# Performance work log

Hardware: AMD Instinct MI355X
Metric: run time of the kernel (lower is better)

The kernel has to match this reference:

```python
import jax, jax.numpy as jnp
import numpy as np


def setup_inputs() -> dict:
    key = jax.random.key(0)
    k1, k2 = jax.random.split(key)
    B, S, H, E = 4, 8192, 4096, 64
    x = jax.random.normal(k1, (B, S, H), dtype=jnp.float32)
    # gate weight [E, H], scaled like a standard init_method
    weight = jax.random.normal(k2, (E, H), dtype=jnp.float32) * (H ** -0.5)
    expert_biases = jnp.zeros((E,), dtype=jnp.float32)
    return {"x": x, "weight": weight, "expert_biases": expert_biases, "top_k": 8}


def reference(x, weight, expert_biases, top_k):
    BIAS_UPDATE_RATE = 0.01
    batch_shape = x.shape[:-1]
    E, H = weight.shape
    flat_x = x.reshape(-1, H)            # [N, H]
    n_tokens = flat_x.shape[0]

    raw_scores = flat_x @ weight.T       # [N, E] gate GEMM
    probs = jax.nn.softmax(raw_scores + expert_biases, axis=-1)  # biased softmax

    expert_weights, expert_indices = jax.lax.top_k(probs, top_k)  # [N, K]

    # bincount with fixed length E (jit-friendly scatter-add)
    token_counts = jnp.zeros((E,), jnp.int32).at[expert_indices.reshape(-1)].add(1)

    # loss-free balancing bias update (training-time buffer update)
    tokens_per_expert = n_tokens * top_k / E
    load_violations = token_counts.astype(jnp.float32) - tokens_per_expert
    new_expert_biases = expert_biases + BIAS_UPDATE_RATE * jnp.sign(load_violations)

    scores = probs.reshape(*batch_shape, E)
    expert_weights = expert_weights.reshape(*batch_shape, top_k)
    expert_indices = expert_indices.reshape(*batch_shape, top_k)
    return (scores, expert_weights, expert_indices, new_expert_biases)
```

## Files before the change

kernel.cpp:

```cpp
#include <hip/hip_runtime.h>

#define NE 64
#define TAU 1e-4f
#define LSTR 68

typedef __bf16 bf16x8 __attribute__((ext_vector_type(8)));
typedef float f32x4 __attribute__((ext_vector_type(4)));

__device__ __forceinline__ void split8(const float4 a0, const float4 a1,
                                       bf16x8& hi, bf16x8& lo) {
  const float xs[8] = {a0.x, a0.y, a0.z, a0.w, a1.x, a1.y, a1.z, a1.w};
#pragma unroll
  for (int i = 0; i < 8; ++i) {
    const __bf16 h = (__bf16)xs[i];
    hi[i] = h;
    lo[i] = (__bf16)(xs[i] - (float)h);
  }
}

__device__ __forceinline__ void gld16(const void* g, void* l) {
  __builtin_amdgcn_global_load_lds(
      (const __attribute__((address_space(1))) void*)g,
      (__attribute__((address_space(3))) void*)l, 16, 0, 0);
}

__global__ void zero512(int* __restrict__ p) { p[threadIdx.x] = 0; }

__global__ __launch_bounds__(256) void wconvert(const float* __restrict__ W,
                                                __bf16* __restrict__ Whi,
                                                __bf16* __restrict__ Wlo,
                                                int n8, int H) {
  const int i = blockIdx.x * 256 + threadIdx.x;
  if (i >= n8) return;
  const int hc = H >> 3;
  const int e = i / hc;
  const int k0 = (i - e * hc) * 8;
  const float4 a0 = *reinterpret_cast<const float4*>(W + (size_t)e * H + k0);
  const float4 a1 =
      *reinterpret_cast<const float4*>(W + (size_t)e * H + k0 + 4);
  bf16x8 hi, lo;
  split8(a0, a1, hi, lo);
  const int tt = k0 >> 5, lk = (k0 >> 3) & 3, j = e >> 4, lr = e & 15;
  const size_t off = (size_t)tt * 2048 + j * 512 + (lk * 16 + lr) * 8;
  *reinterpret_cast<bf16x8*>(Whi + off) = hi;
  *reinterpret_cast<bf16x8*>(Wlo + off) = lo;
}

__global__ __launch_bounds__(512, 2) void gemm_fused(
    const float* __restrict__ X, const __bf16* __restrict__ Whi,
    const __bf16* __restrict__ Wlo, const float* __restrict__ bias,
    float* __restrict__ S, float* __restrict__ wout, float* __restrict__ iout,
    int* __restrict__ cnt, int* __restrict__ hist, int* __restrict__ list,
    int cap, int H, int K) {
  __shared__ alignas(16) char smem[131072];
  __shared__ int hist_s[NE];
  const int tid = threadIdx.x;
  const int lane = tid & 63;
  const int wave = tid >> 6;
  if (tid < NE) hist_s[tid] = 0;
  const int lr = lane & 15;
  const int lk = lane >> 4;
  const int row0 = blockIdx.x * 128;

  __bf16* BH = (__bf16*)smem;
  __bf16* BL = (__bf16*)(smem + 65536);

  const float* xp = X + (size_t)(row0 + 16 * wave + lr) * H + 8 * lk;
  const int T = (H >> 5);
  const int NSL = T >> 4;

  f32x4 acc[4] = {};
  float4 aC0 = *reinterpret_cast<const float4*>(xp);
  float4 aC1 = *reinterpret_cast<const float4*>(xp + 4);

  for (int s = 0; s < NSL; ++s) {
    if (s) __syncthreads();
    const __bf16* sh = Whi + (size_t)s * 32768 + wave * 4096 + lane * 8;
    const __bf16* sl = Wlo + (size_t)s * 32768 + wave * 4096 + lane * 8;
#pragma unroll
    for (int i = 0; i < 8; ++i) {
      gld16(sh + i * 512, BH + wave * 4096 + i * 512);
      gld16(sl + i * 512, BL + wave * 4096 + i * 512);
    }
    asm volatile("s_waitcnt vmcnt(0)" ::: "memory");
    __syncthreads();

#pragma unroll 4
    for (int st = 0; st < 16; ++st) {
      const int t = s * 16 + st;
      const int tn = (t + 1 < T) ? t + 1 : t;
      const float4 aN0 = *reinterpret_cast<const float4*>(xp + 32 * tn);
      const float4 aN1 = *reinterpret_cast<const float4*>(xp + 32 * tn + 4);
      bf16x8 Ahi, Alo;
      split8(aC0, aC1, Ahi, Alo);
      const __bf16* bh = BH + st * 2048 + lane * 8;
      const __bf16* bl = BL + st * 2048 + lane * 8;
      bf16x8 BHf[4], BLf[4];
#pragma unroll
      for (int j = 0; j < 4; ++j) {
        BHf[j] = *reinterpret_cast<const bf16x8*>(bh + j * 512);
        BLf[j] = *reinterpret_cast<const bf16x8*>(bl + j * 512);
      }
#pragma unroll
      for (int j = 0; j < 4; ++j)
        acc[j] = __builtin_amdgcn_mfma_f32_16x16x32_bf16(Alo, BLf[j], acc[j], 0, 0, 0);
#pragma unroll
      for (int j = 0; j < 4; ++j)
        acc[j] = __builtin_amdgcn_mfma_f32_16x16x32_bf16(Alo, BHf[j], acc[j], 0, 0, 0);
#pragma unroll
      for (int j = 0; j < 4; ++j)
        acc[j] = __builtin_amdgcn_mfma_f32_16x16x32_bf16(Ahi, BLf[j], acc[j], 0, 0, 0);
#pragma unroll
      for (int j = 0; j < 4; ++j)
        acc[j] = __builtin_amdgcn_mfma_f32_16x16x32_bf16(Ahi, BHf[j], acc[j], 0, 0, 0);
      aC0 = aN0;
      aC1 = aN1;
    }
  }

  __syncthreads();
  float* Ls = (float*)smem;
#pragma unroll
  for (int j = 0; j < 4; ++j)
#pragma unroll
    for (int r = 0; r < 4; ++r)
      Ls[(16 * wave + 4 * lk + r) * LSTR + 16 * j + lr] = acc[j][r];
  __syncthreads();

  const float bv = bias[lane];
  for (int tt = 0; tt < 16; ++tt) {
    const int tl = wave * 16 + tt;
    const int t = row0 + tl;
    const float s = Ls[tl * LSTR + lane] + bv;

    float m = s;
#pragma unroll
    for (int off = 32; off >= 1; off >>= 1) m = fmaxf(m, __shfl_xor(m, off));
    const float e = expf(s - m);
    float sum = e;
#pragma unroll
    for (int off = 32; off >= 1; off >>= 1) sum += __shfl_xor(sum, off);
    const float p = e / sum;

    float wsel = s;
    float rv = 0.f;
    int ri = 0;
    float prev = 0.f, mingap = 1e30f;
#pragma unroll
    for (int r = 0; r < 9; ++r) {
      float v = wsel;
      int ii = lane;
#pragma unroll
      for (int off = 32; off >= 1; off >>= 1) {
        const float ov = __shfl_xor(v, off);
        const int oi = __shfl_xor(ii, off);
        if (ov > v || (ov == v && oi < ii)) { v = ov; ii = oi; }
      }
      if (r > 0) mingap = fminf(mingap, prev - v);
      prev = v;
      const float pw = __shfl(p, ii);
      if (lane == r) { rv = pw; ri = ii; }
      if (lane == ii) wsel = -1e30f;
    }

    bool toC = false;
    if (mingap < TAU && cap > 0) {
      int pos = 0;
      if (lane == 0) pos = atomicAdd(cnt, 1);
      pos = __shfl(pos, 0);
      if (pos < cap) {
        if (lane == 0) list[pos] = t;
        toC = true;
      }
    }
    if (!toC) {
      S[(size_t)t * NE + lane] = p;
      if (lane < K) {
        wout[(size_t)t * K + lane] = rv;
        iout[(size_t)t * K + lane] = (float)ri;
        atomicAdd(&hist_s[ri], 1);
      }
    }
  }
  __syncthreads();
  if (tid < NE) atomicAdd(&hist[tid], hist_s[tid]);
}

__device__ __forceinline__ void finalize_token_f64(
    int t, int lane, double s, float* __restrict__ S, float* __restrict__ wout,
    float* __restrict__ iout, int* __restrict__ hist, int K) {
  double m = s;
#pragma unroll
  for (int off = 32; off >= 1; off >>= 1) m = fmax(m, __shfl_xor(m, off));
  const double ex = exp(s - m);
  double sum = ex;
#pragma unroll
  for (int off = 32; off >= 1; off >>= 1) sum += __shfl_xor(sum, off);
  const double p = ex / sum;
  S[(size_t)t * NE + lane] = (float)p;
  double wsel = s;
  double rv = 0.0;
  int ri = 0;
  for (int r = 0; r < K; ++r) {
    double v = wsel;
    int ii = lane;
#pragma unroll
    for (int off = 32; off >= 1; off >>= 1) {
      const double ov = __shfl_xor(v, off);
      const int oi = __shfl_xor(ii, off);
      if (ov > v || (ov == v && oi < ii)) { v = ov; ii = oi; }
    }
    const double pw = __shfl(p, ii);
    if (lane == r) { rv = pw; ri = ii; }
    if (lane == ii) wsel = -1e300;
  }
  if (lane < K) {
    wout[(size_t)t * K + lane] = (float)rv;
    iout[(size_t)t * K + lane] = (float)ri;
    atomicAdd(&hist[ri], 1);
  }
}

__global__ __launch_bounds__(256) void recompute_f64(
    const float* __restrict__ X, const float* __restrict__ W,
    const float* __restrict__ bias, float* __restrict__ S,
    float* __restrict__ wout, float* __restrict__ iout,
    const int* __restrict__ cnt, const int* __restrict__ list,
    int* __restrict__ hist, int H, int K, int cap) {
  if (cap <= 0) return;
  __shared__ float4 xs[1024];
  __shared__ double red[256];
  const int tid = threadIdx.x;
  const int n = min(*cnt, cap);
  const int H4 = H >> 2;
  for (int idx = blockIdx.x; idx < n; idx += gridDim.x) {
    const int t = list[idx];
    __syncthreads();
    const float4* xg = reinterpret_cast<const float4*>(X + (size_t)t * H);
    for (int i = tid; i < H4; i += 256) xs[i] = xg[i];
    __syncthreads();
    const int e = tid & 63, sl = tid >> 6;
    const int seg = H4 >> 2;
    const float4* wr =
        reinterpret_cast<const float4*>(W + (size_t)e * H) + (size_t)sl * seg;
    const float4* xr = &xs[sl * seg];
    double a0 = 0.0, a1 = 0.0;
    for (int k = 0; k < seg; k += 2) {
      const float4 w0 = wr[k], w1 = wr[k + 1];
      const float4 v0 = xr[k], v1 = xr[k + 1];
      a0 = fma((double)v0.x, (double)w0.x, a0);
      a0 = fma((double)v0.y, (double)w0.y, a0);
      a0 = fma((double)v0.z, (double)w0.z, a0);
      a0 = fma((double)v0.w, (double)w0.w, a0);
      a1 = fma((double)v1.x, (double)w1.x, a1);
      a1 = fma((double)v1.y, (double)w1.y, a1);
      a1 = fma((double)v1.z, (double)w1.z, a1);
      a1 = fma((double)v1.w, (double)w1.w, a1);
    }
    red[tid] = a0 + a1;
    __syncthreads();
    if (tid < 64) {
      const double s =
          red[e] + red[64 + e] + red[128 + e] + red[192 + e] + (double)bias[e];
      finalize_token_f64(t, e, s, S, wout, iout, hist, K);
    }
  }
}

__global__ void bias_update(const int* __restrict__ hist,
                            const float* __restrict__ bias,
                            float* __restrict__ bout, float tpe) {
  const int e = threadIdx.x;
  const float d = (float)hist[e] - tpe;
  const float sg = (d > 0.f) ? 1.f : ((d < 0.f) ? -1.f : 0.f);
  bout[e] = bias[e] + 0.01f * sg;
}

extern "C" void kernel_launch(void* const* d_in, const int* in_sizes, int n_in,
                              void* d_out, int out_size, void* d_ws, size_t ws_size,
                              hipStream_t stream) {
  const float* x = (const float*)d_in[0];
  const float* w = (const float*)d_in[1];
  const float* bias = (const float*)d_in[2];
  const int E = in_sizes[2];
  const int H = in_sizes[1] / E;
  const long long N = (long long)in_sizes[0] / H;
  const int K = (int)(((long long)out_size - N * E - E) / (2 * N));

  float* S = (float*)d_out;
  float* wout = S + (size_t)N * E;
  float* iout = wout + (size_t)N * K;
  float* bout = iout + (size_t)N * K;

  int* cnt = (int*)d_ws;
  int* hist = (int*)d_ws + 64;
  const size_t whalf = (size_t)E * H * sizeof(__bf16);
  __bf16* Whi = (__bf16*)((char*)d_ws + 4096);
  __bf16* Wlo = (__bf16*)((char*)d_ws + 4096 + whalf);
  const size_t listoff = 4096 + 2 * whalf;
  int* list = (int*)((char*)d_ws + listoff);
  int cap = 0;
  if (ws_size > listoff + 65536)
    cap = (int)min((size_t)32768, (ws_size - listoff) / 4);

  zero512<<<dim3(1), dim3(128), 0, stream>>>((int*)d_ws);
  const int n8 = E * H / 8;
  wconvert<<<dim3((n8 + 255) / 256), 256, 0, stream>>>(w, Whi, Wlo, n8, H);
  gemm_fused<<<dim3((int)(N / 128)), 512, 0, stream>>>(
      x, Whi, Wlo, bias, S, wout, iout, cnt, hist, list, cap, H, K);
  recompute_f64<<<dim3(512), 256, 0, stream>>>(x, w, bias, S, wout, iout, cnt,
                                               list, hist, H, K, cap);
  bias_update<<<dim3(1), dim3(E), 0, stream>>>(hist, bias, bout,
                                               (float)((double)N * K / E));
}
```

Measured before the change: 300.7 us.

## Stage X tiles through LDS with async loads and XOR swizzle, shrink K-slice

```diff
diff --git a/kernel.cpp b/kernel.cpp
--- a/kernel.cpp
+++ b/kernel.cpp
@@ -46,13 +46,13 @@
   *reinterpret_cast<bf16x8*>(Wlo + off) = lo;
 }
 
-__global__ __launch_bounds__(512, 2) void gemm_fused(
+__global__ __launch_bounds__(512, 1) void gemm_fused(
     const float* __restrict__ X, const __bf16* __restrict__ Whi,
     const __bf16* __restrict__ Wlo, const float* __restrict__ bias,
     float* __restrict__ S, float* __restrict__ wout, float* __restrict__ iout,
     int* __restrict__ cnt, int* __restrict__ hist, int* __restrict__ list,
     int cap, int H, int K) {
-  __shared__ alignas(16) char smem[131072];
+  __shared__ alignas(16) char smem[98304];
   __shared__ int hist_s[NE];
   const int tid = threadIdx.x;
   const int lane = tid & 63;
@@ -62,44 +62,53 @@
   const int lk = lane >> 4;
   const int row0 = blockIdx.x * 128;
 
-  __bf16* BH = (__bf16*)smem;
-  __bf16* BL = (__bf16*)(smem + 65536);
-
-  const float* xp = X + (size_t)(row0 + 16 * wave + lr) * H + 8 * lk;
-  const int T = (H >> 5);
-  const int NSL = T >> 4;
+  float* A0 = (float*)smem;
+  __bf16* BH = (__bf16*)(smem + 65536);
+  __bf16* BL = (__bf16*)(smem + 81920);
+
+  const int jj = lane & 31;
+  const int half = lane >> 5;
+  const float* srcA[8];
+#pragma unroll
+  for (int i = 0; i < 8; ++i) {
+    const int r = 2 * i + half;
+    srcA[i] = X + (size_t)(row0 + 16 * wave + r) * H + ((jj ^ (r & 7)) << 2);
+  }
+  const __bf16* srcBh = Whi + wave * 1024 + lane * 8;
+  const __bf16* srcBl = Wlo + wave * 1024 + lane * 8;
 
   f32x4 acc[4] = {};
-  float4 aC0 = *reinterpret_cast<const float4*>(xp);
-  float4 aC1 = *reinterpret_cast<const float4*>(xp + 4);
+  const int NSL = H >> 7;
 
   for (int s = 0; s < NSL; ++s) {
     if (s) __syncthreads();
-    const __bf16* sh = Whi + (size_t)s * 32768 + wave * 4096 + lane * 8;
-    const __bf16* sl = Wlo + (size_t)s * 32768 + wave * 4096 + lane * 8;
-#pragma unroll
-    for (int i = 0; i < 8; ++i) {
-      gld16(sh + i * 512, BH + wave * 4096 + i * 512);
-      gld16(sl + i * 512, BL + wave * 4096 + i * 512);
-    }
+#pragma unroll
+    for (int i = 0; i < 8; ++i)
+      gld16(srcA[i] + s * 128, A0 + wave * 2048 + i * 256);
+    gld16(srcBh + (size_t)s * 8192, BH + wave * 1024);
+    gld16(srcBh + (size_t)s * 8192 + 512, BH + wave * 1024 + 512);
+    gld16(srcBl + (size_t)s * 8192, BL + wave * 1024);
+    gld16(srcBl + (size_t)s * 8192 + 512, BL + wave * 1024 + 512);
     asm volatile("s_waitcnt vmcnt(0)" ::: "memory");
     __syncthreads();
 
-#pragma unroll 4
-    for (int st = 0; st < 16; ++st) {
-      const int t = s * 16 + st;
-      const int tn = (t + 1 < T) ? t + 1 : t;
-      const float4 aN0 = *reinterpret_cast<const float4*>(xp + 32 * tn);
-      const float4 aN1 = *reinterpret_cast<const float4*>(xp + 32 * tn + 4);
+    const float* Aw = A0 + wave * 2048 + lr * 128;
+#pragma unroll
+    for (int ts = 0; ts < 4; ++ts) {
+      const int c0 = (ts << 3) | (lk << 1);
+      const float4 f0 =
+          *reinterpret_cast<const float4*>(Aw + ((c0 ^ (lr & 7)) << 2));
+      const float4 f1 =
+          *reinterpret_cast<const float4*>(Aw + (((c0 + 1) ^ (lr & 7)) << 2));
       bf16x8 Ahi, Alo;
-      split8(aC0, aC1, Ahi, Alo);
-      const __bf16* bh = BH + st * 2048 + lane * 8;
-      const __bf16* bl = BL + st * 2048 + lane * 8;
+      split8(f0, f1, Ahi, Alo);
+      const __bf16* bhp = BH + ts * 2048 + lane * 8;
+      const __bf16* blp = BL + ts * 2048 + lane * 8;
       bf16x8 BHf[4], BLf[4];
 #pragma unroll
       for (int j = 0; j < 4; ++j) {
-        BHf[j] = *reinterpret_cast<const bf16x8*>(bh + j * 512);
-        BLf[j] = *reinterpret_cast<const bf16x8*>(bl + j * 512);
+        BHf[j] = *reinterpret_cast<const bf16x8*>(bhp + j * 512);
+        BLf[j] = *reinterpret_cast<const bf16x8*>(blp + j * 512);
       }
 #pragma unroll
       for (int j = 0; j < 4; ++j)
@@ -113,8 +122,6 @@
 #pragma unroll
       for (int j = 0; j < 4; ++j)
         acc[j] = __builtin_amdgcn_mfma_f32_16x16x32_bf16(Ahi, BHf[j], acc[j], 0, 0, 0);
-      aC0 = aN0;
-      aC1 = aN1;
     }
   }
 
```

Measured after the change: 273.3 us. -9.1%, faster.
